# Kernel tuning notes

Measured on AMD Instinct MI355X. Metric: run time of the kernel, lower is better.

Reference implementation:

```python
import jax, jax.numpy as jnp
import numpy as np

B, C, D, H, W = 4, 1, 192, 192, 192
SMALL = 4            # int(192 * bias_scale=0.025)
BIAS_STD = 0.7
MAX_SIGMA = 3.0
TRUNCATE = 4.0
K = 2 * int(TRUNCATE * MAX_SIGMA) + 1   # fixed truncated kernel size = 25
N_LABELS = 32
TABLE = 128          # static remap-table size (>= max source label, >= max dest)


def setup_inputs() -> dict:
    key = jax.random.key(0)
    k1, k2, k3, k4, k5 = jax.random.split(key, 5)
    return {
        "x": jax.random.normal(k1, (B, C, D, H, W), jnp.float32),
        "small_bias": jax.random.normal(k2, (B, 1, SMALL, SMALL, SMALL), jnp.float32),
        "sigma01": jax.random.uniform(k3, (B, 3), jnp.float32),
        "labels": jax.random.randint(k4, (B, 1, D, H, W), 0, N_LABELS, jnp.int32),
        "source_values": jnp.arange(N_LABELS, dtype=jnp.int64),
        "dest_values": jax.random.randint(k5, (N_LABELS,), 0, 100, jnp.int64),
    }


def _lin_weights(n_in, n_out):
    """Dense 1D linear-interp matrix [n_out, n_in], align_corners=True."""
    pos = jnp.linspace(0.0, n_in - 1.0, n_out)
    i0 = jnp.clip(jnp.floor(pos).astype(jnp.int32), 0, n_in - 2)
    f = pos - i0.astype(pos.dtype)
    r = jnp.arange(n_out)
    Wm = jnp.zeros((n_out, n_in), jnp.float32)
    Wm = Wm.at[r, i0].add(1.0 - f).at[r, i0 + 1].add(f)
    return Wm


def _bias_field(small_bias):
    # trilinear align_corners upsample [B,1,s,s,s] -> [B,1,D,H,W], separable
    b = small_bias * BIAS_STD
    b = jnp.einsum('bcxyz,dx->bcdyz', b, _lin_weights(SMALL, D))
    b = jnp.einsum('bcdyz,hy->bcdhz', b, _lin_weights(SMALL, H))
    b = jnp.einsum('bcdhz,wz->bcdhw', b, _lin_weights(SMALL, W))
    return b


def _gauss_kernels(sigma):
    """sigma [3] -> normalized kernels [3, K]; identity (delta) where sigma<0.01."""
    ar = jnp.arange(K, dtype=jnp.float32) - K // 2
    s = jnp.maximum(sigma, 1e-3)[:, None]
    g = jnp.exp(-0.5 * (ar[None, :] ** 2) / (s ** 2))
    g = g / g.sum(-1, keepdims=True)
    delta = jnp.zeros((K,), jnp.float32).at[K // 2].set(1.0)
    return jnp.where(sigma[:, None] >= 0.01, g, delta[None, :])


def _blur_axis(x, k, axis):
    # x [C,D,H,W]; depthwise 1D conv along `axis` with replicate (edge) padding
    p = K // 2
    xm = jnp.moveaxis(x, axis, -1)
    shp = xm.shape
    xm = xm.reshape(-1, 1, shp[-1])
    xm = jnp.pad(xm, ((0, 0), (0, 0), (p, p)), mode='edge')
    out = jax.lax.conv_general_dilated(xm, k.reshape(1, 1, K), (1,), 'VALID')
    return jnp.moveaxis(out.reshape(shp), -1, axis)


def _blur_sample(x, kernels):
    # x [C,D,H,W], kernels [3,K]; separable blur over D,H,W
    for i, ax in enumerate((1, 2, 3)):
        x = _blur_axis(x, kernels[i], ax)
    return x


def reference(x, small_bias, sigma01, labels, source_values, dest_values):
    # 1) bias-field corruption: x * exp(upsampled random field)
    img = x * jnp.exp(_bias_field(small_bias))
    # 2) dynamic per-sample Gaussian blur, sigma in [0, MAX_SIGMA]
    kernels = jax.vmap(_gauss_kernels)(sigma01 * MAX_SIGMA)   # [B,3,K]
    img = jax.vmap(_blur_sample)(img, kernels)
    # 3) label remap via lookup table gather
    mapping = jnp.zeros((TABLE,), jnp.int32).at[source_values].set(
        dest_values.astype(jnp.int32))
    labels_out = mapping[labels]
    return img, labels_out
```

## Files before the change

### kernel.cpp

```cpp
#include <hip/hip_runtime.h>
#include <hip/hip_fp16.h>
#include <cstdint>
#include <cstddef>

#define Bc 4
#define Dd 192
#define Hh 192
#define Ww 192
#define KK 25
#define RR 12
#define VOL (Bc*Dd*Hh*Ww)
#define SP 216
#define SPU (SP/2)
#define SH 98
#define RIN 56
#define RD  56

typedef unsigned short u16;
typedef unsigned int   u32;
typedef __fp16 h2 __attribute__((ext_vector_type(2)));

__device__ inline u32 pk2(float a, float b) {
    return __builtin_bit_cast(u32, __builtin_amdgcn_cvt_pkrtz(a, b));
}

__global__ void setup_tables_kernel(const float* __restrict__ sigma01,
                                    const int* __restrict__ src,
                                    const int* __restrict__ dst,
                                    u32* __restrict__ kern2,
                                    int* __restrict__ mapping,
                                    float* __restrict__ mapf) {
    int t = threadIdx.x;
    if (t < 128) mapping[t] = 0;
    __syncthreads();
    if (t < 32) {
        int s = src[t];
        if (s >= 0 && s < 128) mapping[s] = dst[t];
    }
    __syncthreads();
    if (t < 128) mapf[t] = (float)mapping[t];
    if (t < Bc * 3) {
        float sig = sigma01[t] * 3.0f;
        float s = fmaxf(sig, 1e-3f);
        float g[KK];
        float sum = 0.0f;
        #pragma unroll
        for (int i = 0; i < KK; i++) {
            float a = (float)(i - RR);
            float v = expf(-0.5f * a * a / (s * s));
            g[i] = v; sum += v;
        }
        float inv = 1.0f / sum;
        #pragma unroll
        for (int i = 0; i < KK; i++) {
            float v = g[i] * inv;
            if (sig < 0.01f) v = (i == RR) ? 1.0f : 0.0f;
            u16 hb = __builtin_bit_cast(u16, __float2half(v));
            kern2[t * KK + i] = (u32)hb | ((u32)hb << 16);
        }
    }
}

__global__ __launch_bounds__(256, 6) void pass_wh_remap_kernel(
    const float* __restrict__ x, u16* __restrict__ outB,
    const u32* __restrict__ kern2, const float* __restrict__ sb,
    const int4* __restrict__ labels, float4* __restrict__ lab_out,
    const float* __restrict__ mapf) {
    __shared__ u16 P[RIN * SP];
    __shared__ float2 ch2[RIN * 3];
    const int tid = threadIdx.x;
    const int hx = blockIdx.x;
    const int d  = blockIdx.y;
    const int b  = blockIdx.z;

    if (tid < RIN) {
        int r = tid;
        int hrow = min(max(32 * hx - RR + r, 0), Hh - 1);
        float pos_d = d * (3.0f / 191.0f);
        int   id0   = min((int)pos_d, 2);
        float fd    = pos_d - (float)id0;
        float pos_h = hrow * (3.0f / 191.0f);
        int   ih0   = min((int)pos_h, 2);
        float fh    = pos_h - (float)ih0;
        const float* sbA = sb + b * 64 + id0 * 16 + ih0 * 4;
        float c[4];
        #pragma unroll
        for (int k = 0; k < 4; k++) {
            float v00 = sbA[k],      v01 = sbA[4 + k];
            float v10 = sbA[16 + k], v11 = sbA[20 + k];
            float vd0 = (1.f - fd) * v00 + fd * v10;
            float vd1 = (1.f - fd) * v01 + fd * v11;
            c[k] = ((1.f - fh) * vd0 + fh * vd1) * 0.7f;
        }
        #pragma unroll
        for (int k = 0; k < 3; k++)
            ch2[r * 3 + k] = make_float2(c[k], c[k + 1] - c[k]);
    }
    __syncthreads();

    const size_t pbase = ((size_t)b * Dd + d) * (size_t)(Hh * Ww);
    #pragma unroll
    for (int it = 0; it < 11; it++) {
        int i4 = it * 256 + tid;
        if (i4 < RIN * 48) {
            int r = i4 / 48, w4 = i4 % 48;
            int w = 4 * w4;
            int hrow = min(max(32 * hx - RR + r, 0), Hh - 1);
            float4 v = *(const float4*)(x + pbase + (size_t)hrow * Ww + w);
            float rs[4];
            #pragma unroll
            for (int j = 0; j < 4; j++) {
                float pw = (float)(w + j) * (3.0f / 191.0f);
                int sel = (pw >= 1.0f) + (pw >= 2.0f);
                float2 cd = ch2[r * 3 + sel];
                float bias = fmaf(pw - (float)sel, cd.y, cd.x);
                float val = (j == 0 ? v.x : j == 1 ? v.y : j == 2 ? v.z : v.w);
                rs[j] = val * __expf(bias);
            }
            u32* dstp = (u32*)&P[r * SP + RR + w];
            dstp[0] = pk2(rs[0], rs[1]);
            dstp[1] = pk2(rs[2], rs[3]);
            if (w4 == 0) {
                u32 hh = pk2(rs[0], rs[0]);
                u32* hp = (u32*)&P[r * SP];
                #pragma unroll
                for (int m = 0; m < 6; m++) hp[m] = hh;
            } else if (w4 == 47) {
                u32 hh = pk2(rs[3], rs[3]);
                u32* hp = (u32*)&P[r * SP + RR + Ww];
                #pragma unroll
                for (int m = 0; m < 6; m++) hp[m] = hh;
            }
        }
    }
    __syncthreads();

    {
        const int bid = (b * Dd + d) * 6 + hx;
        const int4* lp = labels + (size_t)bid * 1536 + tid;
        int4 lab[6];
        #pragma unroll
        for (int m = 0; m < 6; m++) lab[m] = lp[m * 256];
        float4* op = lab_out + (size_t)bid * 1536 + tid;
        #pragma unroll
        for (int m = 0; m < 6; m++) {
            int4 l = lab[m];
            float4 o;
            o.x = mapf[min(max(l.x, 0), 127)];
            o.y = mapf[min(max(l.y, 0), 127)];
            o.z = mapf[min(max(l.z, 0), 127)];
            o.w = mapf[min(max(l.w, 0), 127)];
            op[m * 256] = o;
        }
    }

    {
        const u32* kw2 = kern2 + (b * 3 + 2) * KK;
        const int wv = tid >> 6, ln = tid & 63;
        const int r4 = ln >> 4;
        const int c  = ln & 15;
        #pragma unroll
        for (int it = 0; it < 4; it++) {
            const int lr = it * 4 + r4;
            if (lr < 14) {
                const int row = wv * 14 + lr;
                const u32* rp = (const u32*)P + row * SPU + 6 * c;
                u32 E[18];
                #pragma unroll
                for (int j = 0; j < 18; j++) E[j] = rp[j];
                u32 O[17];
                #pragma unroll
                for (int j = 0; j < 17; j++)
                    O[j] = (E[j] >> 16) | (E[j + 1] << 16);
                h2 acc[6];
                #pragma unroll
                for (int m = 0; m < 6; m++) acc[m] = (h2)(0.0f);
                #pragma unroll
                for (int s = 0; s < 13; s++) {
                    h2 kv = __builtin_bit_cast(h2, kw2[2 * s]);
                    #pragma unroll
                    for (int m = 0; m < 6; m++)
                        acc[m] += kv * __builtin_bit_cast(h2, E[m + s]);
                }
                #pragma unroll
                for (int s = 0; s < 12; s++) {
                    h2 kv = __builtin_bit_cast(h2, kw2[2 * s + 1]);
                    #pragma unroll
                    for (int m = 0; m < 6; m++)
                        acc[m] += kv * __builtin_bit_cast(h2, O[m + s]);
                }
                u32* wp = (u32*)P + row * SPU + 6 + 6 * c;
                #pragma unroll
                for (int m = 0; m < 6; m++)
                    wp[m] = __builtin_bit_cast(u32, acc[m]);
            }
        }
    }
    __syncthreads();

    {
        const u32* kh2 = kern2 + (b * 3 + 1) * KK;
        u32* outp = (u32*)(outB + pbase);
        #pragma unroll
        for (int it = 0; it < 3; it++) {
            int item = it * 256 + tid;
            int col = item % 96;
            int g = item / 96;
            u32 win[28];
            #pragma unroll
            for (int i = 0; i < 28; i++)
                win[i] = *((const u32*)P + (g * 4 + i) * SPU + 6 + col);
            h2 acc[4];
            #pragma unroll
            for (int j = 0; j < 4; j++) acc[j] = (h2)(0.0f);
            #pragma unroll
            for (int t = 0; t < KK; t++) {
                h2 kv = __builtin_bit_cast(h2, kh2[t]);
                #pragma unroll
                for (int j = 0; j < 4; j++)
                    acc[j] += kv * __builtin_bit_cast(h2, win[j + t]);
            }
            #pragma unroll
            for (int j = 0; j < 4; j++)
                outp[(32 * hx + g * 4 + j) * 96 + col] =
                    __builtin_bit_cast(u32, acc[j]);
        }
    }
}

__global__ __launch_bounds__(192) void pass_d_kernel(
    const u16* __restrict__ in, float* __restrict__ img,
    const u32* __restrict__ kern2) {
    __shared__ __attribute__((aligned(16))) u16 T[RD * SH];
    const int tid = threadIdx.x;
    const int w0 = blockIdx.x * 96;
    const int d0 = blockIdx.y * 32;
    const int z = blockIdx.z;
    const int h = z % Hh, b = z / Hh;
    const u32* kp = kern2 + b * 3 * KK;
    #pragma unroll
    for (int k = 0; k < 4; k++) {
        int idx = k * 192 + tid;
        if (idx < RD * 12) {
            int r = idx / 12, sg = idx % 12;
            int dd = min(max(d0 + r - RR, 0), Dd - 1);
            uint4 v = *(const uint4*)(in + (((size_t)b * Dd + dd) * Hh + h) * (size_t)Ww + w0 + sg * 8);
            u32* p = (u32*)&T[r * SH + sg * 8];
            p[0] = v.x; p[1] = v.y; p[2] = v.z; p[3] = v.w;
        }
    }
    __syncthreads();
    const int p = tid % 48;
    const int g = tid / 48;
    const int ob = g * 8;
    u32 win[32];
    #pragma unroll
    for (int i = 0; i < 32; i++) win[i] = *(const u32*)&T[(ob + i) * SH + 2 * p];
    h2 acc[8];
    #pragma unroll
    for (int j = 0; j < 8; j++) acc[j] = (h2)(0.0f);
    #pragma unroll
    for (int t = 0; t < KK; t++) {
        h2 kv = __builtin_bit_cast(h2, kp[t]);
        #pragma unroll
        for (int j = 0; j < 8; j++)
            acc[j] += kv * __builtin_bit_cast(h2, win[j + t]);
    }
    #pragma unroll
    for (int j = 0; j < 8; j++) {
        h2 a = acc[j];
        float2 f = make_float2((float)a.x, (float)a.y);
        *(float2*)(img + (((size_t)b * Dd + (d0 + ob + j)) * Hh + h) * (size_t)Ww + w0 + 2 * p) = f;
    }
}

extern "C" void kernel_launch(void* const* d_in, const int* in_sizes, int n_in,
                              void* d_out, int out_size, void* d_ws, size_t ws_size,
                              hipStream_t stream) {
    const float* x          = (const float*)d_in[0];
    const float* small_bias = (const float*)d_in[1];
    const float* sigma01    = (const float*)d_in[2];
    const int*   labels     = (const int*)d_in[3];
    const int*   src        = (const int*)d_in[4];
    const int*   dst        = (const int*)d_in[5];

    float* out     = (float*)d_out;
    float* img     = out;
    float* lab_out = out + (size_t)VOL;

    u32*   kern2   = (u32*)((float*)d_ws + 384);
    int*   mapping = (int*)((float*)d_ws + 768);
    float* mapf    = (float*)d_ws + 896;
    u16*   Bb      = (u16*)((char*)d_ws + 8192);

    setup_tables_kernel<<<1, 128, 0, stream>>>(sigma01, src, dst, kern2,
                                               mapping, mapf);

    pass_wh_remap_kernel<<<dim3(6, Dd, Bc), 256, 0, stream>>>(
        x, Bb, kern2, small_bias,
        (const int4*)labels, (float4*)lab_out, mapf);
    pass_d_kernel<<<dim3(Ww / 96, Dd / 32, Bc * Hh), 192, 0, stream>>>(Bb, img, kern2);
}
```

Baseline: 138.8 us.

## Compute W-axis blur with MFMA Toeplitz matmul into separate LDS buffer

```diff
diff --git a/kernel.cpp b/kernel.cpp
--- a/kernel.cpp
+++ b/kernel.cpp
@@ -12,6 +12,7 @@
 #define VOL (Bc*Dd*Hh*Ww)
 #define SP 216
 #define SPU (SP/2)
+#define S2 200
 #define SH 98
 #define RIN 56
 #define RD  56
@@ -19,6 +20,8 @@
 typedef unsigned short u16;
 typedef unsigned int   u32;
 typedef __fp16 h2 __attribute__((ext_vector_type(2)));
+typedef __fp16 h8 __attribute__((ext_vector_type(8)));
+typedef float  f32x4 __attribute__((ext_vector_type(4)));
 
 __device__ inline u32 pk2(float a, float b) {
     return __builtin_bit_cast(u32, __builtin_amdgcn_cvt_pkrtz(a, b));
@@ -61,13 +64,15 @@
     }
 }
 
-__global__ __launch_bounds__(256, 6) void pass_wh_remap_kernel(
+__global__ __launch_bounds__(256) void pass_wh_remap_kernel(
     const float* __restrict__ x, u16* __restrict__ outB,
     const u32* __restrict__ kern2, const float* __restrict__ sb,
     const int4* __restrict__ labels, float4* __restrict__ lab_out,
     const float* __restrict__ mapf) {
     __shared__ u16 P[RIN * SP];
+    __shared__ u16 P2[RIN * S2];
     __shared__ float2 ch2[RIN * 3];
+    __shared__ u16 kpadW[64];
     const int tid = threadIdx.x;
     const int hx = blockIdx.x;
     const int d  = blockIdx.y;
@@ -95,6 +100,13 @@
         #pragma unroll
         for (int k = 0; k < 3; k++)
             ch2[r * 3 + k] = make_float2(c[k], c[k + 1] - c[k]);
+    }
+    if (tid >= 64 && tid < 128) {
+        int i = tid - 64;
+        int t = i - 15;
+        u16 v = (t >= 0 && t < KK) ? (u16)(kern2[(b * 3 + 2) * KK + t] & 0xFFFFu)
+                                   : (u16)0;
+        kpadW[i] = v;
     }
     __syncthreads();
 
@@ -155,44 +167,34 @@
     }
 
     {
-        const u32* kw2 = kern2 + (b * 3 + 2) * KK;
-        const int wv = tid >> 6, ln = tid & 63;
-        const int r4 = ln >> 4;
+        const int ln = tid & 63, wv = tid >> 6;
         const int c  = ln & 15;
-        #pragma unroll
-        for (int it = 0; it < 4; it++) {
-            const int lr = it * 4 + r4;
-            if (lr < 14) {
-                const int row = wv * 14 + lr;
-                const u32* rp = (const u32*)P + row * SPU + 6 * c;
-                u32 E[18];
-                #pragma unroll
-                for (int j = 0; j < 18; j++) E[j] = rp[j];
-                u32 O[17];
-                #pragma unroll
-                for (int j = 0; j < 17; j++)
-                    O[j] = (E[j] >> 16) | (E[j + 1] << 16);
-                h2 acc[6];
-                #pragma unroll
-                for (int m = 0; m < 6; m++) acc[m] = (h2)(0.0f);
-                #pragma unroll
-                for (int s = 0; s < 13; s++) {
-                    h2 kv = __builtin_bit_cast(h2, kw2[2 * s]);
-                    #pragma unroll
-                    for (int m = 0; m < 6; m++)
-                        acc[m] += kv * __builtin_bit_cast(h2, E[m + s]);
-                }
-                #pragma unroll
-                for (int s = 0; s < 12; s++) {
-                    h2 kv = __builtin_bit_cast(h2, kw2[2 * s + 1]);
-                    #pragma unroll
-                    for (int m = 0; m < 6; m++)
-                        acc[m] += kv * __builtin_bit_cast(h2, O[m + s]);
-                }
-                u32* wp = (u32*)P + row * SPU + 6 + 6 * c;
-                #pragma unroll
-                for (int m = 0; m < 6; m++)
-                    wp[m] = __builtin_bit_cast(u32, acc[m]);
+        const int kg = ln >> 4;
+        h8 B0, B1;
+        #pragma unroll
+        for (int j = 0; j < 8; j++) {
+            int k = kg * 8 + j;
+            B0[j] = __builtin_bit_cast(__fp16, kpadW[15 + k - c]);
+            int i1 = 15 + k + 32 - c;
+            B1[j] = __builtin_bit_cast(__fp16, (i1 < 64) ? kpadW[i1] : (u16)0);
+        }
+        const int ra = min(wv * 16 + c, RIN - 1);
+        const int rd0 = wv * 16 + kg * 4;
+        #pragma unroll
+        for (int ct = 0; ct < 12; ct++) {
+            const u16* ap = &P[ra * SP + ct * 16 + kg * 8];
+            const u16* ap1 = (kg == 0) ? ap + 32 : ap;
+            h8 A0 = __builtin_bit_cast(h8, *(const uint4*)ap);
+            h8 A1 = __builtin_bit_cast(h8, *(const uint4*)ap1);
+            f32x4 acc = {0.f, 0.f, 0.f, 0.f};
+            acc = __builtin_amdgcn_mfma_f32_16x16x32_f16(A0, B0, acc, 0, 0, 0);
+            acc = __builtin_amdgcn_mfma_f32_16x16x32_f16(A1, B1, acc, 0, 0, 0);
+            #pragma unroll
+            for (int m = 0; m < 4; m++) {
+                int rd = rd0 + m;
+                if (rd < RIN)
+                    P2[rd * S2 + ct * 16 + c] =
+                        __builtin_bit_cast(u16, (__fp16)acc[m]);
             }
         }
     }
@@ -209,7 +211,7 @@
             u32 win[28];
             #pragma unroll
             for (int i = 0; i < 28; i++)
-                win[i] = *((const u32*)P + (g * 4 + i) * SPU + 6 + col);
+                win[i] = *((const u32*)P2 + (g * 4 + i) * (S2 / 2) + col);
             h2 acc[4];
             #pragma unroll
             for (int j = 0; j < 4; j++) acc[j] = (h2)(0.0f);
```

Result: slower. 160.4 us (+15.6%).
